# Kernel tuning notes

Hardware: AMD Instinct MI355X
Metric: run time of the kernel (lower is better)

## Reference

```python
import jax, jax.numpy as jnp
import numpy as np

B, T, F, UNITS, OUT_STEPS = 512, 128, 64, 1024, 32


def setup_inputs() -> dict:
    key = jax.random.key(0)
    k0, k1, k2, k3 = jax.random.split(key, 4)
    return {
        "inputs": jax.random.normal(k0, (B, T, F), jnp.float32),
        "Wk": jax.random.normal(k1, (F, 4 * UNITS), jnp.float32) * 0.02,   # input kernel (i,f,c,o)
        "Wr": jax.random.normal(k2, (UNITS, 4 * UNITS), jnp.float32) * 0.02,  # recurrent kernel
        "b": jnp.zeros((4 * UNITS,), jnp.float32),
        "Wd": jax.random.normal(k3, (UNITS, F), jnp.float32) * 0.02,  # output Dense
        "bd": jnp.zeros((F,), jnp.float32),
        "out_steps": OUT_STEPS,
    }


def _lstm_cell(h, c, x, Wk, Wr, b):
    # Keras LSTMCell: z packed as (i, f, g, o); sigmoid gates, tanh cell.
    z = x @ Wk + h @ Wr + b
    i, f, g, o = jnp.split(z, 4, axis=-1)
    c = jax.nn.sigmoid(f) * c + jax.nn.sigmoid(i) * jnp.tanh(g)
    h = jax.nn.sigmoid(o) * jnp.tanh(c)
    return h, c


def reference(inputs, Wk, Wr, b, Wd, bd, out_steps):
    Bn = inputs.shape[0]
    units = Wr.shape[0]
    h0 = jnp.zeros((Bn, units), inputs.dtype)
    c0 = jnp.zeros((Bn, units), inputs.dtype)

    # warmup: run LSTM over the input window, keep final state
    def warm(carry, x_t):
        h, c = carry
        h, c = _lstm_cell(h, c, x_t, Wk, Wr, b)
        return (h, c), None

    (h, c), _ = jax.lax.scan(warm, (h0, c0), jnp.swapaxes(inputs, 0, 1))
    pred0 = h @ Wd + bd  # first-step prediction [B, F]

    def dec(carry, _):
        pred, h, c = carry
        h, c = _lstm_cell(h, c, pred, Wk, Wr, b)
        pred = h @ Wd + bd
        return (pred, h, c), pred

    _, rest = jax.lax.scan(dec, (pred0, h, c), None, length=out_steps - 1)
    preds = jnp.concatenate([pred0[None], rest], axis=0)  # [out_steps, B, F]
    return jnp.transpose(preds, (1, 0, 2))  # [B, out_steps, F]
```

## Files before the change

### kernel.cpp

```cpp
#include <hip/hip_runtime.h>
#include <math.h>

#define BATCH 512
#define TT    128
#define FF    64
#define UU    1024
#define ZZ    4096
#define OS    32
#define KTOT  1088
#define NCH   17
#define CROW  72
#define CBUF  (64 * CROW)
#define NKB   68

typedef _Float16 f16x8 __attribute__((ext_vector_type(8)));
typedef float f32x16 __attribute__((ext_vector_type(16)));

__device__ __forceinline__ float sigf(float x) { return 1.0f / (1.0f + expf(-x)); }

__global__ __launch_bounds__(256) void wconv(
    const float* __restrict__ Wk, const float* __restrict__ Wr,
    _Float16* __restrict__ WT)
{
    __shared__ float T[32][129];
    const int k0 = blockIdx.x * 32;
    const int n0 = blockIdx.y * 128;
    const int u0 = n0 >> 2;
    const int t = threadIdx.x;
    #pragma unroll
    for (int i = 0; i < 16; ++i) {
        int idx = t + i * 256;
        int u = idx & 31, k = (idx >> 5) & 31, g = idx >> 10;
        int krow = k0 + k;
        int col = g * UU + u0 + u;
        float wv = (krow < FF) ? Wk[(size_t)krow * ZZ + col]
                               : Wr[(size_t)(krow - FF) * ZZ + col];
        T[k][u * 4 + g] = wv;
    }
    __syncthreads();
    #pragma unroll
    for (int i = 0; i < 16; ++i) {
        int idx = t + i * 256;
        int k = idx & 31, np = idx >> 5;
        int r = n0 + np;
        int kk = k0 + k;
        size_t o = ((size_t)(r >> 5) * NKB + (kk >> 4)) * 512
                 + (size_t)((((kk >> 3) & 1) * 32 + (r & 31)) * 8 + (kk & 7));
        WT[o] = (_Float16)T[k][np];
    }
}

__global__ __launch_bounds__(256) void init_k(
    uint4* __restrict__ zbase, const float* __restrict__ x0,
    _Float16* __restrict__ xF)
{
    const int b = blockIdx.x, t = threadIdx.x;
    if (b < 768) {
        zbase[(size_t)b * 256 + t] = make_uint4(0u, 0u, 0u, 0u);
    } else {
        int e = (b - 768) * 256 + t;
        int bb = e >> 6, f = e & 63;
        xF[e] = (_Float16)x0[(size_t)bb * (TT * FF) + f];
    }
}

__global__ __launch_bounds__(512, 2) void lstm_cell_mfma(
    const _Float16* __restrict__ xF,
    const _Float16* __restrict__ hF,
    _Float16* __restrict__ hFo,
    float* __restrict__ c,
    const _Float16* __restrict__ WT,
    const float* __restrict__ bias,
    const float* __restrict__ xnext, _Float16* __restrict__ xnF)
{
    __shared__ __align__(16) char smem[64 * 132 * 4];
    _Float16* lds = (_Float16*)smem;
    float* z = (float*)smem;

    const int t = threadIdx.x;
    const int lane = t & 63;
    const int w  = t >> 6;
    const int mw = w >> 2;
    const int nw = w & 3;
    const int n0 = blockIdx.x * 128;
    const int r0 = blockIdx.y * 64;
    const int u0 = n0 >> 2;
    const int l31 = lane & 31;

    const int srow = t >> 3;
    const int sseg = t & 7;
    const _Float16* aAx = xF + (size_t)(r0 + srow) * FF + sseg * 8;
    const _Float16* aAh = hF + (size_t)(r0 + srow) * UU + sseg * 8;
    const int wA = srow * CROW + sseg * 8;
    uint4 sA[2];

    const _Float16* pW = WT + ((size_t)(blockIdx.x * 4 + nw) * NKB) * 512 + lane * 8;

    const int fra = (mw * 32 + l31) * CROW + (lane >> 5) * 8;

    f32x16 acc;
    #pragma unroll
    for (int i = 0; i < 16; ++i) acc[i] = 0.f;

    f16x8 wf[3][4];

#define LOADA(ch)                                                              \
    {                                                                          \
        sA[(ch) & 1] = ((ch) == 0) ? *(const uint4*)aAx                        \
                                   : *(const uint4*)(aAh + ((ch) - 1) * 64);   \
    }
#define LOADW(ch)                                                              \
    {                                                                          \
        _Pragma("unroll")                                                      \
        for (int s = 0; s < 4; ++s)                                            \
            wf[(ch) % 3][s] = *(const f16x8*)(pW + ((ch) * 4 + s) * 512);      \
    }
#define WRITEA(ch)                                                             \
    {                                                                          \
        *(uint4*)(lds + ((ch) & 1) * CBUF + wA) = sA[(ch) & 1];                \
    }

    LOADA(0)
    LOADW(0)
    LOADA(1)
    LOADW(1)
    WRITEA(0)

    #pragma unroll
    for (int ch = 0; ch < NCH; ++ch) {
        if (ch + 2 < NCH) { LOADA(ch + 2) LOADW(ch + 2) }
        __builtin_amdgcn_s_waitcnt(0xC07F);
        __builtin_amdgcn_s_barrier();
        if (ch + 1 < NCH) WRITEA(ch + 1)
        const _Float16* b = lds + (ch & 1) * CBUF;
        #pragma unroll
        for (int s = 0; s < 4; ++s) {
            f16x8 af = *(const f16x8*)(b + fra + s * 16);
            acc = __builtin_amdgcn_mfma_f32_32x32x16_f16(af, wf[ch % 3][s], acc, 0, 0, 0);
        }
    }
#undef LOADA
#undef LOADW
#undef WRITEA

    __syncthreads();

    {
        const int nloc = nw * 32 + l31;
        const int gs = (nloc & 3) * 33 + (nloc >> 2);
        const int rbase = mw * 32 + 4 * (lane >> 5);
        #pragma unroll
        for (int r = 0; r < 16; ++r) {
            int m = rbase + (r & 3) + 8 * (r >> 2);
            z[m * 132 + gs] = acc[r];
        }
    }
    __syncthreads();

    {
        const int ul = t & 31;
        const int uu = u0 + ul;
        const float bi = bias[uu], bfr = bias[UU + uu];
        const float bg = bias[2 * UU + uu], bo = bias[3 * UU + uu];
        #pragma unroll
        for (int rep = 0; rep < 4; ++rep) {
            int m = (t >> 5) * 4 + rep;
            float zi = z[m * 132 + ul];
            float zf = z[m * 132 + 33 + ul];
            float zg = z[m * 132 + 66 + ul];
            float zo = z[m * 132 + 99 + ul];
            size_t idx = (size_t)(r0 + m) * UU + uu;
            float cn = sigf(zf + bfr) * c[idx] + sigf(zi + bi) * tanhf(zg + bg);
            c[idx] = cn;
            hFo[idx] = (_Float16)(sigf(zo + bo) * tanhf(cn));
        }
    }

    if (xnext != nullptr && t < 128) {
        int e = (blockIdx.x + 32 * blockIdx.y) * 128 + t;
        int bb = e >> 6, f = e & 63;
        xnF[e] = (_Float16)xnext[(size_t)bb * (TT * FF) + f];
    }
}

__global__ __launch_bounds__(256) void dense_out(
    const _Float16* __restrict__ hF,
    const float* __restrict__ Wd, const float* __restrict__ bd,
    _Float16* __restrict__ pF, float* __restrict__ outp)
{
    __shared__ float red[4][64];
    const int t = threadIdx.x, f = t & 63, ks = t >> 6, bb = blockIdx.x;
    const f16x8* hr = (const f16x8*)(hF + (size_t)bb * UU + ks * 256);
    const float* wp = Wd + (size_t)(ks * 256) * FF + f;
    float s = 0.f;
    #pragma unroll 4
    for (int v = 0; v < 32; ++v) {
        f16x8 a = hr[v];
        #pragma unroll
        for (int j = 0; j < 8; ++j)
            s += (float)a[j] * wp[(size_t)(v * 8 + j) * FF];
    }
    red[ks][f] = s;
    __syncthreads();
    if (ks == 0) {
        float vv = red[0][f] + red[1][f] + red[2][f] + red[3][f] + bd[f];
        outp[(size_t)bb * (OS * FF) + f] = vv;
        pF[bb * FF + f] = (_Float16)vv;
    }
}

extern "C" void kernel_launch(void* const* d_in, const int* in_sizes, int n_in,
                              void* d_out, int out_size, void* d_ws, size_t ws_size,
                              hipStream_t stream) {
    const float* inputs = (const float*)d_in[0];
    const float* Wk     = (const float*)d_in[1];
    const float* Wr     = (const float*)d_in[2];
    const float* bias   = (const float*)d_in[3];
    const float* Wd     = (const float*)d_in[4];
    const float* bd     = (const float*)d_in[5];
    float* out = (float*)d_out;

    char* ws = (char*)d_ws;
    _Float16* hF0 = (_Float16*)(ws);
    float*    cb  = (float*)(ws + 1048576);
    _Float16* hF1 = (_Float16*)(ws + 3145728);
    _Float16* WT  = (_Float16*)(ws + 4194304);
    _Float16* x0F = (_Float16*)(ws + 13107200);
    _Float16* x1F = (_Float16*)(ws + 13172736);
    _Float16* prF = (_Float16*)(ws + 13238272);

    wconv<<<dim3(34, 32), 256, 0, stream>>>(Wk, Wr, WT);
    init_k<<<896, 256, 0, stream>>>((uint4*)ws, inputs, x0F);

    dim3 cgrid(32, 8);
    _Float16 *hc = hF0, *hn = hF1;

    for (int t = 0; t < TT; ++t) {
        const _Float16* xF = (t & 1) ? x1F : x0F;
        _Float16* xnF = (t & 1) ? x0F : x1F;
        const float* xnext = (t < TT - 1) ? (inputs + (size_t)(t + 1) * FF) : nullptr;
        lstm_cell_mfma<<<cgrid, 512, 0, stream>>>(xF, hc, hn, cb, WT, bias, xnext, xnF);
        _Float16* tp = hc; hc = hn; hn = tp;
    }

    dense_out<<<BATCH, 256, 0, stream>>>(hc, Wd, bd, prF, out);

    for (int s = 1; s < OS; ++s) {
        lstm_cell_mfma<<<cgrid, 512, 0, stream>>>(prF, hc, hn, cb, WT, bias, nullptr, nullptr);
        _Float16* tp = hc; hc = hn; hn = tp;
        dense_out<<<BATCH, 256, 0, stream>>>(hc, Wd, bd, prF, out + (size_t)s * FF);
    }
}
```

Measured before the change: 2.696 ms.

## Fold dense output into recurrent weights for decode and fuse dense into cell kernel

Precomputes Wr + Wd·Wk and b + bd·Wk so that decode steps multiply only h (K=1024) instead of [pred, h]. This removes the serial dense kernel from the decode chain. The dense output for the previous step is now computed by extra blocks inside the same cell kernel launch, and a final dense kernel handles the last step. Weight prefetch depth also goes from two to three chunks. The price is one more fused-weight buffer and setup kernel. Rounding also changes, because pred is no longer quantised to fp16 before feeding back.

```diff
diff --git a/kernel.cpp b/kernel.cpp
--- a/kernel.cpp
+++ b/kernel.cpp
@@ -8,10 +8,12 @@
 #define ZZ    4096
 #define OS    32
 #define KTOT  1088
-#define NCH   17
+#define NCHW  17
+#define NCHD  16
 #define CROW  72
 #define CBUF  (64 * CROW)
-#define NKB   68
+#define NKBW  68
+#define NKBD  64
 
 typedef _Float16 f16x8 __attribute__((ext_vector_type(8)));
 typedef float f32x16 __attribute__((ext_vector_type(16)));
@@ -42,12 +44,61 @@
     for (int i = 0; i < 16; ++i) {
         int idx = t + i * 256;
         int k = idx & 31, np = idx >> 5;
-        int r = n0 + np;
-        int kk = k0 + k;
-        size_t o = ((size_t)(r >> 5) * NKB + (kk >> 4)) * 512
+        int r = n0 + np, kk = k0 + k;
+        size_t o = ((size_t)(r >> 5) * NKBW + (kk >> 4)) * 512
                  + (size_t)((((kk >> 3) & 1) * 32 + (r & 31)) * 8 + (kk & 7));
         WT[o] = (_Float16)T[k][np];
     }
+}
+
+__global__ __launch_bounds__(256) void wfus(
+    const float* __restrict__ Wk, const float* __restrict__ Wr,
+    const float* __restrict__ Wd, _Float16* __restrict__ WT2)
+{
+    __shared__ float Wkk[64][128];
+    __shared__ float Wdd[32][65];
+    const int k0 = blockIdx.x * 32;
+    const int n0 = blockIdx.y * 128;
+    const int u0 = n0 >> 2;
+    const int t = threadIdx.x;
+    #pragma unroll
+    for (int i = 0; i < 32; ++i) {
+        int idx = t + i * 256;
+        int f = idx >> 7, np = idx & 127;
+        int col = (np & 3) * UU + u0 + (np >> 2);
+        Wkk[f][np] = Wk[(size_t)f * ZZ + col];
+    }
+    #pragma unroll
+    for (int i = 0; i < 8; ++i) {
+        int idx = t + i * 256;
+        int k = idx >> 6, f = idx & 63;
+        Wdd[k][f] = Wd[(size_t)(k0 + k) * FF + f];
+    }
+    __syncthreads();
+    #pragma unroll 1
+    for (int i = 0; i < 16; ++i) {
+        int idx = t + i * 256;
+        int k = idx & 31, np = idx >> 5;
+        int col = (np & 3) * UU + u0 + (np >> 2);
+        float v = Wr[(size_t)(k0 + k) * ZZ + col];
+        #pragma unroll
+        for (int f = 0; f < 64; ++f) v += Wdd[k][f] * Wkk[f][np];
+        int r = n0 + np, kk = k0 + k;
+        size_t o = ((size_t)(r >> 5) * NKBD + (kk >> 4)) * 512
+                 + (size_t)((((kk >> 3) & 1) * 32 + (r & 31)) * 8 + (kk & 7));
+        WT2[o] = (_Float16)v;
+    }
+}
+
+__global__ __launch_bounds__(256) void bfus(
+    const float* __restrict__ Wk, const float* __restrict__ b,
+    const float* __restrict__ bd, float* __restrict__ b2)
+{
+    int col = blockIdx.x * 256 + threadIdx.x;
+    float v = b[col];
+    #pragma unroll 8
+    for (int f = 0; f < 64; ++f) v += bd[f] * Wk[(size_t)f * ZZ + col];
+    b2[col] = v;
 }
 
 __global__ __launch_bounds__(256) void init_k(
@@ -64,13 +115,10 @@
     }
 }
 
-__global__ __launch_bounds__(512, 2) void lstm_cell_mfma(
-    const _Float16* __restrict__ xF,
-    const _Float16* __restrict__ hF,
-    _Float16* __restrict__ hFo,
-    float* __restrict__ c,
-    const _Float16* __restrict__ WT,
-    const float* __restrict__ bias,
+__global__ __launch_bounds__(512, 2) void cell_warm(
+    const _Float16* __restrict__ xF, const _Float16* __restrict__ hF,
+    _Float16* __restrict__ hFo, float* __restrict__ c,
+    const _Float16* __restrict__ WT, const float* __restrict__ bias,
     const float* __restrict__ xnext, _Float16* __restrict__ xnF)
 {
     __shared__ __align__(16) char smem[64 * 132 * 4];
@@ -80,29 +128,25 @@
     const int t = threadIdx.x;
     const int lane = t & 63;
     const int w  = t >> 6;
-    const int mw = w >> 2;
-    const int nw = w & 3;
+    const int mw = w >> 2, nw = w & 3;
     const int n0 = blockIdx.x * 128;
     const int r0 = blockIdx.y * 64;
     const int u0 = n0 >> 2;
     const int l31 = lane & 31;
 
-    const int srow = t >> 3;
-    const int sseg = t & 7;
+    const int srow = t >> 3, sseg = t & 7;
     const _Float16* aAx = xF + (size_t)(r0 + srow) * FF + sseg * 8;
     const _Float16* aAh = hF + (size_t)(r0 + srow) * UU + sseg * 8;
     const int wA = srow * CROW + sseg * 8;
     uint4 sA[2];
 
-    const _Float16* pW = WT + ((size_t)(blockIdx.x * 4 + nw) * NKB) * 512 + lane * 8;
-
+    const _Float16* pW = WT + ((size_t)(blockIdx.x * 4 + nw) * NKBW) * 512 + lane * 8;
     const int fra = (mw * 32 + l31) * CROW + (lane >> 5) * 8;
 
     f32x16 acc;
     #pragma unroll
     for (int i = 0; i < 16; ++i) acc[i] = 0.f;
-
-    f16x8 wf[3][4];
+    f16x8 wf[4][4];
 
 #define LOADA(ch)                                                              \
     {                                                                          \
@@ -113,30 +157,29 @@
     {                                                                          \
         _Pragma("unroll")                                                      \
         for (int s = 0; s < 4; ++s)                                            \
-            wf[(ch) % 3][s] = *(const f16x8*)(pW + ((ch) * 4 + s) * 512);      \
+            wf[(ch) & 3][s] = *(const f16x8*)(pW + ((ch) * 4 + s) * 512);      \
     }
 #define WRITEA(ch)                                                             \
     {                                                                          \
         *(uint4*)(lds + ((ch) & 1) * CBUF + wA) = sA[(ch) & 1];                \
     }
 
-    LOADA(0)
-    LOADW(0)
-    LOADA(1)
-    LOADW(1)
+    LOADA(0) LOADW(0)
+    LOADA(1) LOADW(1) LOADW(2)
     WRITEA(0)
 
     #pragma unroll
-    for (int ch = 0; ch < NCH; ++ch) {
-        if (ch + 2 < NCH) { LOADA(ch + 2) LOADW(ch + 2) }
+    for (int ch = 0; ch < NCHW; ++ch) {
+        if (ch + 2 < NCHW) LOADA(ch + 2)
+        if (ch + 3 < NCHW) LOADW(ch + 3)
         __builtin_amdgcn_s_waitcnt(0xC07F);
         __builtin_amdgcn_s_barrier();
-        if (ch + 1 < NCH) WRITEA(ch + 1)
+        if (ch + 1 < NCHW) WRITEA(ch + 1)
         const _Float16* b = lds + (ch & 1) * CBUF;
         #pragma unroll
         for (int s = 0; s < 4; ++s) {
             f16x8 af = *(const f16x8*)(b + fra + s * 16);
-            acc = __builtin_amdgcn_mfma_f32_32x32x16_f16(af, wf[ch % 3][s], acc, 0, 0, 0);
+            acc = __builtin_amdgcn_mfma_f32_32x32x16_f16(af, wf[ch & 3][s], acc, 0, 0, 0);
         }
     }
 #undef LOADA
@@ -144,7 +187,6 @@
 #undef WRITEA
 
     __syncthreads();
-
     {
         const int nloc = nw * 32 + l31;
         const int gs = (nloc & 3) * 33 + (nloc >> 2);
@@ -156,7 +198,6 @@
         }
     }
     __syncthreads();
-
     {
         const int ul = t & 31;
         const int uu = u0 + ul;
@@ -175,7 +216,6 @@
             hFo[idx] = (_Float16)(sigf(zo + bo) * tanhf(cn));
         }
     }
-
     if (xnext != nullptr && t < 128) {
         int e = (blockIdx.x + 32 * blockIdx.y) * 128 + t;
         int bb = e >> 6, f = e & 63;
@@ -183,30 +223,144 @@
     }
 }
 
-__global__ __launch_bounds__(256) void dense_out(
-    const _Float16* __restrict__ hF,
-    const float* __restrict__ Wd, const float* __restrict__ bd,
-    _Float16* __restrict__ pF, float* __restrict__ outp)
-{
-    __shared__ float red[4][64];
-    const int t = threadIdx.x, f = t & 63, ks = t >> 6, bb = blockIdx.x;
-    const f16x8* hr = (const f16x8*)(hF + (size_t)bb * UU + ks * 256);
-    const float* wp = Wd + (size_t)(ks * 256) * FF + f;
-    float s = 0.f;
-    #pragma unroll 4
-    for (int v = 0; v < 32; ++v) {
-        f16x8 a = hr[v];
-        #pragma unroll
-        for (int j = 0; j < 8; ++j)
-            s += (float)a[j] * wp[(size_t)(v * 8 + j) * FF];
-    }
-    red[ks][f] = s;
-    __syncthreads();
-    if (ks == 0) {
-        float vv = red[0][f] + red[1][f] + red[2][f] + red[3][f] + bd[f];
-        outp[(size_t)bb * (OS * FF) + f] = vv;
-        pF[bb * FF + f] = (_Float16)vv;
-    }
+__device__ __forceinline__ void dense_step(
+    const _Float16* __restrict__ hF, const float* __restrict__ Wd,
+    const float* __restrict__ bd, float* __restrict__ outp,
+    char* smem, int rbase)
+{
+    float* red = (float*)smem;
+    const int t = threadIdx.x, f = t & 63, ks = t >> 6;
+    const _Float16* hb = hF + (size_t)rbase * UU + ks * 128;
+    const float* wp = Wd + (size_t)(ks * 128) * FF + f;
+    float s[8] = {0.f, 0.f, 0.f, 0.f, 0.f, 0.f, 0.f, 0.f};
+    #pragma unroll 2
+    for (int v = 0; v < 16; ++v) {
+        f16x8 a[8];
+        #pragma unroll
+        for (int r = 0; r < 8; ++r) a[r] = *(const f16x8*)(hb + r * UU + v * 8);
+        #pragma unroll
+        for (int j = 0; j < 8; ++j) {
+            float wv = wp[(size_t)(v * 8 + j) * FF];
+            #pragma unroll
+            for (int r = 0; r < 8; ++r) s[r] += (float)a[r][j] * wv;
+        }
+    }
+    #pragma unroll
+    for (int r = 0; r < 8; ++r) red[(ks * 8 + r) * 64 + f] = s[r];
+    __syncthreads();
+    {
+        const int r = t >> 6;
+        float vv = bd[f];
+        #pragma unroll
+        for (int k = 0; k < 8; ++k) vv += red[(k * 8 + r) * 64 + f];
+        outp[(size_t)(rbase + r) * (OS * FF) + f] = vv;
+    }
+}
+
+__global__ __launch_bounds__(512, 2) void cell_dec(
+    const _Float16* __restrict__ hF, _Float16* __restrict__ hFo,
+    float* __restrict__ c, const _Float16* __restrict__ WT2,
+    const float* __restrict__ b2, const float* __restrict__ Wd,
+    const float* __restrict__ bd, float* __restrict__ outp)
+{
+    __shared__ __align__(16) char smem[64 * 132 * 4];
+    if (blockIdx.x >= 256) {
+        dense_step(hF, Wd, bd, outp, smem, (blockIdx.x - 256) * 8);
+        return;
+    }
+    _Float16* lds = (_Float16*)smem;
+    float* z = (float*)smem;
+
+    const int t = threadIdx.x;
+    const int lane = t & 63;
+    const int w  = t >> 6;
+    const int mw = w >> 2, nw = w & 3;
+    const int panel = blockIdx.x & 31, rtile = blockIdx.x >> 5;
+    const int n0 = panel * 128, r0 = rtile * 64, u0 = n0 >> 2;
+    const int l31 = lane & 31;
+
+    const int srow = t >> 3, sseg = t & 7;
+    const _Float16* aAh = hF + (size_t)(r0 + srow) * UU + sseg * 8;
+    const int wA = srow * CROW + sseg * 8;
+    uint4 sA[2];
+
+    const _Float16* pW = WT2 + ((size_t)(panel * 4 + nw) * NKBD) * 512 + lane * 8;
+    const int fra = (mw * 32 + l31) * CROW + (lane >> 5) * 8;
+
+    f32x16 acc;
+    #pragma unroll
+    for (int i = 0; i < 16; ++i) acc[i] = 0.f;
+    f16x8 wf[4][4];
+
+#define LOADA(ch)  { sA[(ch) & 1] = *(const uint4*)(aAh + (ch) * 64); }
+#define LOADW(ch)                                                              \
+    {                                                                          \
+        _Pragma("unroll")                                                      \
+        for (int s = 0; s < 4; ++s)                                            \
+            wf[(ch) & 3][s] = *(const f16x8*)(pW + ((ch) * 4 + s) * 512);      \
+    }
+#define WRITEA(ch) { *(uint4*)(lds + ((ch) & 1) * CBUF + wA) = sA[(ch) & 1]; }
+
+    LOADA(0) LOADW(0)
+    LOADA(1) LOADW(1) LOADW(2)
+    WRITEA(0)
+
+    #pragma unroll
+    for (int ch = 0; ch < NCHD; ++ch) {
+        if (ch + 2 < NCHD) LOADA(ch + 2)
+        if (ch + 3 < NCHD) LOADW(ch + 3)
+        __builtin_amdgcn_s_waitcnt(0xC07F);
+        __builtin_amdgcn_s_barrier();
+        if (ch + 1 < NCHD) WRITEA(ch + 1)
+        const _Float16* b = lds + (ch & 1) * CBUF;
+        #pragma unroll
+        for (int s = 0; s < 4; ++s) {
+            f16x8 af = *(const f16x8*)(b + fra + s * 16);
+            acc = __builtin_amdgcn_mfma_f32_32x32x16_f16(af, wf[ch & 3][s], acc, 0, 0, 0);
+        }
+    }
+#undef LOADA
+#undef LOADW
+#undef WRITEA
+
+    __syncthreads();
+    {
+        const int nloc = nw * 32 + l31;
+        const int gs = (nloc & 3) * 33 + (nloc >> 2);
+        const int rbase = mw * 32 + 4 * (lane >> 5);
+        #pragma unroll
+        for (int r = 0; r < 16; ++r) {
+            int m = rbase + (r & 3) + 8 * (r >> 2);
+            z[m * 132 + gs] = acc[r];
+        }
+    }
+    __syncthreads();
+    {
+        const int ul = t & 31;
+        const int uu = u0 + ul;
+        const float bi = b2[uu], bfr = b2[UU + uu];
+        const float bg = b2[2 * UU + uu], bo = b2[3 * UU + uu];
+        #pragma unroll
+        for (int rep = 0; rep < 4; ++rep) {
+            int m = (t >> 5) * 4 + rep;
+            float zi = z[m * 132 + ul];
+            float zf = z[m * 132 + 33 + ul];
+            float zg = z[m * 132 + 66 + ul];
+            float zo = z[m * 132 + 99 + ul];
+            size_t idx = (size_t)(r0 + m) * UU + uu;
+            float cn = sigf(zf + bfr) * c[idx] + sigf(zi + bi) * tanhf(zg + bg);
+            c[idx] = cn;
+            hFo[idx] = (_Float16)(sigf(zo + bo) * tanhf(cn));
+        }
+    }
+}
+
+__global__ __launch_bounds__(512) void dense_fin(
+    const _Float16* __restrict__ hF, const float* __restrict__ Wd,
+    const float* __restrict__ bd, float* __restrict__ outp)
+{
+    __shared__ __align__(16) char smem[16384];
+    dense_step(hF, Wd, bd, outp, smem, blockIdx.x * 8);
 }
 
 extern "C" void kernel_launch(void* const* d_in, const int* in_sizes, int n_in,
@@ -225,11 +379,14 @@
     float*    cb  = (float*)(ws + 1048576);
     _Float16* hF1 = (_Float16*)(ws + 3145728);
     _Float16* WT  = (_Float16*)(ws + 4194304);
-    _Float16* x0F = (_Float16*)(ws + 13107200);
-    _Float16* x1F = (_Float16*)(ws + 13172736);
-    _Float16* prF = (_Float16*)(ws + 13238272);
+    _Float16* WT2 = (_Float16*)(ws + 13107200);
+    _Float16* x0F = (_Float16*)(ws + 21495808);
+    _Float16* x1F = (_Float16*)(ws + 21561344);
+    float*    b2  = (float*)(ws + 21626880);
 
     wconv<<<dim3(34, 32), 256, 0, stream>>>(Wk, Wr, WT);
+    wfus<<<dim3(32, 32), 256, 0, stream>>>(Wk, Wr, Wd, WT2);
+    bfus<<<16, 256, 0, stream>>>(Wk, bias, bd, b2);
     init_k<<<896, 256, 0, stream>>>((uint4*)ws, inputs, x0F);
 
     dim3 cgrid(32, 8);
@@ -239,15 +396,14 @@
         const _Float16* xF = (t & 1) ? x1F : x0F;
         _Float16* xnF = (t & 1) ? x0F : x1F;
         const float* xnext = (t < TT - 1) ? (inputs + (size_t)(t + 1) * FF) : nullptr;
-        lstm_cell_mfma<<<cgrid, 512, 0, stream>>>(xF, hc, hn, cb, WT, bias, xnext, xnF);
+        cell_warm<<<cgrid, 512, 0, stream>>>(xF, hc, hn, cb, WT, bias, xnext, xnF);
         _Float16* tp = hc; hc = hn; hn = tp;
     }
 
-    dense_out<<<BATCH, 256, 0, stream>>>(hc, Wd, bd, prF, out);
-
     for (int s = 1; s < OS; ++s) {
-        lstm_cell_mfma<<<cgrid, 512, 0, stream>>>(prF, hc, hn, cb, WT, bias, nullptr, nullptr);
+        cell_dec<<<320, 512, 0, stream>>>(hc, hn, cb, WT2, b2, Wd, bd,
+                                          out + (size_t)(s - 1) * FF);
         _Float16* tp = hc; hc = hn; hn = tp;
-        dense_out<<<BATCH, 256, 0, stream>>>(hc, Wd, bd, prF, out + (size_t)s * FF);
-    }
-}
+    }
+    dense_fin<<<64, 512, 0, stream>>>(hc, Wd, bd, out + (size_t)(OS - 1) * FF);
+}
```

Result: no change. 2.723 ms (+1.0%).
